# Optimization experiments

Measured on AMD Instinct MI355X. Metric: run time of the kernel, lower is better.

Reference implementation:

```python
import jax, jax.numpy as jnp
import numpy as np

H = 16  # text_transformer_heads


def setup_inputs() -> dict:
    key = jax.random.key(0)
    ks = jax.random.split(key, 5)
    B, T, D = 2, 2048, 1024
    std = D ** -0.5
    return {
        "x": jax.random.normal(ks[0], (B, T, D), dtype=jnp.float32),
        "wq": jax.random.normal(ks[1], (D, D), dtype=jnp.float32) * std,
        "bq": jnp.zeros((D,), dtype=jnp.float32),
        "wk": jax.random.normal(ks[2], (D, D), dtype=jnp.float32) * std,
        "bk": jnp.zeros((D,), dtype=jnp.float32),
        "wv": jax.random.normal(ks[3], (D, D), dtype=jnp.float32) * std,
        "bv": jnp.zeros((D,), dtype=jnp.float32),
        "wo": jax.random.normal(ks[4], (D, D), dtype=jnp.float32) * std,
        "bo": jnp.zeros((D,), dtype=jnp.float32),
    }


def reference(x, wq, bq, wk, bk, wv, bv, wo, bo):
    # Faithful to the original: masked_fill result was discarded in torch,
    # so NO causal mask is applied; scale is 1/sqrt(T) (seq len, not head dim).
    B, T, D = x.shape
    hd = D // H
    q = (x @ wq.T + bq).reshape(B, T, H, hd).transpose(0, 2, 1, 3)  # [B,H,T,hd]
    k = (x @ wk.T + bk).reshape(B, T, H, hd).transpose(0, 2, 1, 3)
    v = (x @ wv.T + bv).reshape(B, T, H, hd).transpose(0, 2, 1, 3)
    scores = jnp.einsum("bhqd,bhkd->bhqk", q, k) / jnp.sqrt(jnp.float32(T))
    attn = jax.nn.softmax(scores, axis=-1)
    ctx = jnp.einsum("bhqk,bhkd->bhqd", attn, v)
    ctx = ctx.transpose(0, 2, 1, 3).reshape(B, T, D)
    return ctx @ wo.T + bo
```

## Files before the change

### kernel.cpp

```cpp
#include <hip/hip_runtime.h>
#include <hip/hip_bf16.h>
#include <stdint.h>

typedef __bf16 bf16x8_t __attribute__((ext_vector_type(8)));
typedef float f32x4_t __attribute__((ext_vector_type(4)));

#define B_SZ 2
#define T_SZ 2048
#define D_SZ 1024
#define H_SZ 16
#define M_SZ 4096
#define QK_SCALE (0.02209708691207961f * 1.4426950408889634f)

__device__ __forceinline__ void gld_lds16(const void* g, void* l) {
  __builtin_amdgcn_global_load_lds(
      (const __attribute__((address_space(1))) unsigned int*)g,
      (__attribute__((address_space(3))) unsigned int*)l, 16, 0, 0);
}

__device__ __forceinline__ int xcd_swz(int bid, int nwg) {
  return (bid & 7) * (nwg >> 3) + (bid >> 3);
}

__global__ __launch_bounds__(256) void cast_all_k(
    const float* __restrict__ x, const float* __restrict__ wq,
    const float* __restrict__ wk, const float* __restrict__ wv,
    const float* __restrict__ wo, __hip_bfloat16* __restrict__ dst) {
  size_t i = ((size_t)blockIdx.x * 256 + threadIdx.x) * 4;
  if (i >= 8388608) return;
  const float* src;
  size_t off;
  if (i < 4194304) { src = x; off = i; }
  else {
    size_t r = i - 4194304;
    int s = (int)(r >> 20);
    off = r & 1048575;
    src = s == 0 ? wq : s == 1 ? wk : s == 2 ? wv : wo;
  }
  float4 v = *(const float4*)(src + off);
  __hip_bfloat16 h0 = __float2bfloat16(v.x), h1 = __float2bfloat16(v.y);
  __hip_bfloat16 h2 = __float2bfloat16(v.z), h3 = __float2bfloat16(v.w);
  ushort4 u;
  u.x = *(unsigned short*)&h0; u.y = *(unsigned short*)&h1;
  u.z = *(unsigned short*)&h2; u.w = *(unsigned short*)&h3;
  *(ushort4*)(dst + i) = u;
}

__device__ __forceinline__ void gemm_mainloop(
    const __hip_bfloat16* __restrict__ A, const __hip_bfloat16* __restrict__ W,
    int m0, int n0, __hip_bfloat16* a_lds, __hip_bfloat16* b_lds,
    f32x4_t (&acc)[4][4]) {
  const int tid = threadIdx.x;
  const int w = tid >> 6, l = tid & 63, lr = l & 15, lg = l >> 4;
  const int wm = w >> 1, wn = w & 1;
  const int c0 = tid, c1 = tid + 256;
  const int r0 = c0 >> 2, k0c = c0 & 3;
  const int r1 = c1 >> 2, k1c = c1 & 3;
  const __hip_bfloat16* ga0 = A + (size_t)(m0 + r0) * 1024 + 8 * (k0c ^ (r0 & 3));
  const __hip_bfloat16* ga1 = A + (size_t)(m0 + r1) * 1024 + 8 * (k1c ^ (r1 & 3));
  const __hip_bfloat16* gb0 = W + (size_t)(n0 + r0) * 1024 + 8 * (k0c ^ (r0 & 3));
  const __hip_bfloat16* gb1 = W + (size_t)(n0 + r1) * 1024 + 8 * (k1c ^ (r1 & 3));
  __hip_bfloat16* la0 = a_lds + w * 512;
  __hip_bfloat16* la1 = a_lds + 2048 + w * 512;
  __hip_bfloat16* lb0 = b_lds + w * 512;
  __hip_bfloat16* lb1 = b_lds + 2048 + w * 512;

  int aoff[4], boff[4];
#pragma unroll
  for (int f = 0; f < 4; ++f) {
    int ra = wm * 64 + f * 16 + lr;
    aoff[f] = ra * 32 + 8 * (lg ^ (ra & 3));
    int rb = wn * 64 + f * 16 + lr;
    boff[f] = rb * 32 + 8 * (lg ^ (rb & 3));
  }

  for (int kk = 0; kk < 1024; kk += 32) {
    gld_lds16(ga0 + kk, la0);
    gld_lds16(ga1 + kk, la1);
    gld_lds16(gb0 + kk, lb0);
    gld_lds16(gb1 + kk, lb1);
    __syncthreads();
    bf16x8_t af[4], bfr[4];
#pragma unroll
    for (int f = 0; f < 4; ++f) {
      af[f]  = *(const bf16x8_t*)(a_lds + aoff[f]);
      bfr[f] = *(const bf16x8_t*)(b_lds + boff[f]);
    }
#pragma unroll
    for (int i = 0; i < 4; ++i)
#pragma unroll
      for (int j = 0; j < 4; ++j)
        acc[i][j] = __builtin_amdgcn_mfma_f32_16x16x32_bf16(af[i], bfr[j], acc[i][j], 0, 0, 0);
    __syncthreads();
  }
}

__global__ __launch_bounds__(256, 2) void gemm_qkv(
    const __hip_bfloat16* __restrict__ xb,
    const __hip_bfloat16* __restrict__ wqb, const __hip_bfloat16* __restrict__ wkb,
    const __hip_bfloat16* __restrict__ wvb,
    const float* __restrict__ bq, const float* __restrict__ bk,
    const float* __restrict__ bv,
    __hip_bfloat16* __restrict__ qo, __hip_bfloat16* __restrict__ ko,
    __hip_bfloat16* __restrict__ vto) {
  __shared__ __hip_bfloat16 a_lds[4096];
  __shared__ __hip_bfloat16 b_lds[4096];
  const int lin = xcd_swz(blockIdx.y * 24 + blockIdx.x, 768);
  const int bx = lin % 24, by = lin / 24;
  const int n0g = bx * 128;
  const int m0  = by * 128;
  const int seg = n0g >> 10;
  const int n0  = n0g & 1023;
  const __hip_bfloat16* W = seg == 0 ? wqb : seg == 1 ? wkb : wvb;
  const float* bias = seg == 0 ? bq : seg == 1 ? bk : bv;

  f32x4_t acc[4][4] = {};
  gemm_mainloop(xb, W, m0, n0, a_lds, b_lds, acc);

  const int tid = threadIdx.x;
  const int w = tid >> 6, l = tid & 63, lr = l & 15, lg = l >> 4;
  const int wm = w >> 1, wn = w & 1;
#pragma unroll
  for (int i = 0; i < 4; ++i) {
#pragma unroll
    for (int j = 0; j < 4; ++j) {
      const int col = n0 + wn * 64 + j * 16 + lr;
      const float bb = bias[col];
      f32x4_t v = acc[i][j];
      const int row0 = m0 + wm * 64 + i * 16 + lg * 4;
      if (seg == 0) {
#pragma unroll
        for (int e = 0; e < 4; ++e)
          qo[(size_t)(row0 + e) * 1024 + col] = __float2bfloat16((v[e] + bb) * QK_SCALE);
      } else if (seg == 1) {
#pragma unroll
        for (int e = 0; e < 4; ++e)
          ko[(size_t)(row0 + e) * 1024 + col] = __float2bfloat16(v[e] + bb);
      } else {
        const int h = col >> 6, d = col & 63;
        const int b = row0 >> 11, t0 = row0 & 2047;
        union { unsigned short s[4]; uint2 u; } pk;
#pragma unroll
        for (int e = 0; e < 4; ++e) {
          __hip_bfloat16 hv = __float2bfloat16(v[e] + bb);
          pk.s[e] = *(unsigned short*)&hv;
        }
        *(uint2*)(vto + ((size_t)((b * 16 + h) * 64 + d)) * 2048 + t0) = pk.u;
      }
    }
  }
}

__global__ __launch_bounds__(512, 4) void attn_k(
    const __hip_bfloat16* __restrict__ q, const __hip_bfloat16* __restrict__ k,
    const __hip_bfloat16* __restrict__ vt, __hip_bfloat16* __restrict__ ctx) {
  __shared__ __hip_bfloat16 k_lds[2][4096];
  __shared__ __hip_bfloat16 v_lds[2][4096];
  __shared__ __hip_bfloat16 p_lds[8192];
  const int tid = threadIdx.x, w = tid >> 6, l = tid & 63;
  const int lr = l & 15, lg = l >> 4;
  const int bh = blockIdx.y, b = bh >> 4, h = bh & 15;
  const int q0 = blockIdx.x * 128;

  const int srow = tid >> 3, scc = tid & 7;
  const __hip_bfloat16* ksrc = k + ((size_t)(b * T_SZ + srow)) * 1024 + h * 64 + 8 * (scc ^ (srow & 7));
  const __hip_bfloat16* vsrc = vt + ((size_t)(bh * 64 + srow)) * 2048 + 8 * (scc ^ (srow & 7));
  __hip_bfloat16* kdst0 = &k_lds[0][0] + w * 512;
  __hip_bfloat16* kdst1 = &k_lds[1][0] + w * 512;
  __hip_bfloat16* vdst0 = &v_lds[0][0] + w * 512;
  __hip_bfloat16* vdst1 = &v_lds[1][0] + w * 512;
  __hip_bfloat16* pw = p_lds + w * 1024;

  gld_lds16(ksrc, kdst0);
  gld_lds16(vsrc, vdst0);

  const size_t qbase = ((size_t)(b * T_SZ + q0 + w * 16 + lr)) * 1024 + h * 64 + 8 * lg;
  const bf16x8_t aQ0 = *(const bf16x8_t*)(q + qbase);
  const bf16x8_t aQ1 = *(const bf16x8_t*)(q + qbase + 32);

  float mrow = -1e30f, lrow = 0.f;
  f32x4_t acc[4] = {};

  auto tile = [&](const __hip_bfloat16* kr, const __hip_bfloat16* vr,
                  bool pf, int tn, __hip_bfloat16* kd, __hip_bfloat16* vd) {
    if (pf) {
      gld_lds16(ksrc + (size_t)tn * 64 * 1024, kd);
      gld_lds16(vsrc + tn * 64, vd);
      asm volatile("s_waitcnt vmcnt(2)" ::: "memory");
    } else {
      asm volatile("s_waitcnt vmcnt(0)" ::: "memory");
    }
    __builtin_amdgcn_s_barrier();
    asm volatile("" ::: "memory");

    f32x4_t sf[4];
#pragma unroll
    for (int nt = 0; nt < 4; ++nt) {
      const int row = nt * 16 + lr;
      bf16x8_t b0 = *(const bf16x8_t*)(kr + row * 64 + 8 * (lg ^ (row & 7)));
      bf16x8_t b1 = *(const bf16x8_t*)(kr + row * 64 + 8 * ((lg + 4) ^ (row & 7)));
      f32x4_t s = {};
      s = __builtin_amdgcn_mfma_f32_16x16x32_bf16(b0, aQ0, s, 0, 0, 0);
      s = __builtin_amdgcn_mfma_f32_16x16x32_bf16(b1, aQ1, s, 0, 0, 0);
      sf[nt] = s;
    }

    float tmax = sf[0][0];
#pragma unroll
    for (int nt = 0; nt < 4; ++nt)
#pragma unroll
      for (int e = 0; e < 4; ++e) tmax = fmaxf(tmax, sf[nt][e]);
    tmax = fmaxf(tmax, __shfl_xor(tmax, 16));
    tmax = fmaxf(tmax, __shfl_xor(tmax, 32));
    const float newm = fmaxf(mrow, tmax);
    const float sc = __builtin_amdgcn_exp2f(mrow - newm);
    float rsum = 0.f;
#pragma unroll
    for (int nt = 0; nt < 4; ++nt)
#pragma unroll
      for (int e = 0; e < 4; ++e) {
        float p = __builtin_amdgcn_exp2f(sf[nt][e] - newm);
        sf[nt][e] = p;
        rsum += p;
      }
    rsum += __shfl_xor(rsum, 16);
    rsum += __shfl_xor(rsum, 32);
    lrow = lrow * sc + rsum;
    mrow = newm;

#pragma unroll
    for (int nt = 0; nt < 4; ++nt) {
      union { unsigned short s[4]; uint2 u; } pk;
#pragma unroll
      for (int e = 0; e < 4; ++e) {
        __hip_bfloat16 hv = __float2bfloat16(sf[nt][e]);
        pk.s[e] = *(unsigned short*)&hv;
      }
      const int off = lr * 64 + 8 * ((nt * 2 + (lg >> 1)) ^ (lr & 7)) + (lg & 1) * 4;
      *(uint2*)(pw + off) = pk.u;
    }

    float sce[4];
#pragma unroll
    for (int e = 0; e < 4; ++e) sce[e] = __shfl(sc, lg * 4 + e, 16);
#pragma unroll
    for (int dt = 0; dt < 4; ++dt)
#pragma unroll
      for (int e = 0; e < 4; ++e) acc[dt][e] *= sce[e];

    asm volatile("s_waitcnt lgkmcnt(0)" ::: "memory");
    const bf16x8_t aP0 = *(const bf16x8_t*)(pw + lr * 64 + 8 * (lg ^ (lr & 7)));
    const bf16x8_t aP1 = *(const bf16x8_t*)(pw + lr * 64 + 8 * ((lg + 4) ^ (lr & 7)));

#pragma unroll
    for (int dt = 0; dt < 4; ++dt) {
      const int drow = dt * 16 + lr;
      bf16x8_t bv0 = *(const bf16x8_t*)(vr + drow * 64 + 8 * (lg ^ (drow & 7)));
      bf16x8_t bv1 = *(const bf16x8_t*)(vr + drow * 64 + 8 * ((lg + 4) ^ (drow & 7)));
      acc[dt] = __builtin_amdgcn_mfma_f32_16x16x32_bf16(aP0, bv0, acc[dt], 0, 0, 0);
      acc[dt] = __builtin_amdgcn_mfma_f32_16x16x32_bf16(aP1, bv1, acc[dt], 0, 0, 0);
    }
    asm volatile("" ::: "memory");
    __builtin_amdgcn_s_barrier();
  };

  const __hip_bfloat16* kb0 = &k_lds[0][0];
  const __hip_bfloat16* kb1 = &k_lds[1][0];
  const __hip_bfloat16* vb0 = &v_lds[0][0];
  const __hip_bfloat16* vb1 = &v_lds[1][0];
#pragma unroll 1
  for (int p = 0; p < 16; ++p) {
    tile(kb0, vb0, true, 2 * p + 1, kdst1, vdst1);
    tile(kb1, vb1, p < 15, 2 * p + 2, kdst0, vdst0);
  }

  const float inv = 1.0f / lrow;
  float inve[4];
#pragma unroll
  for (int e = 0; e < 4; ++e) inve[e] = __shfl(inv, lg * 4 + e, 16);
#pragma unroll
  for (int e = 0; e < 4; ++e) {
    const int row = q0 + w * 16 + lg * 4 + e;
#pragma unroll
    for (int dt = 0; dt < 4; ++dt) {
      const int d = dt * 16 + lr;
      ctx[((size_t)(b * T_SZ + row)) * 1024 + h * 64 + d] =
          __float2bfloat16(acc[dt][e] * inve[e]);
    }
  }
}

__global__ __launch_bounds__(256, 2) void gemm_out(
    const __hip_bfloat16* __restrict__ ctx, const __hip_bfloat16* __restrict__ wob,
    const float* __restrict__ bo, float* __restrict__ out) {
  __shared__ __hip_bfloat16 a_lds[4096];
  __shared__ __hip_bfloat16 b_lds[4096];
  const int lin = xcd_swz(blockIdx.y * 8 + blockIdx.x, 256);
  const int n0 = (lin % 8) * 128, m0 = (lin / 8) * 128;
  f32x4_t acc[4][4] = {};
  gemm_mainloop(ctx, wob, m0, n0, a_lds, b_lds, acc);
  const int tid = threadIdx.x;
  const int w = tid >> 6, l = tid & 63, lr = l & 15, lg = l >> 4;
  const int wm = w >> 1, wn = w & 1;
#pragma unroll
  for (int i = 0; i < 4; ++i) {
#pragma unroll
    for (int j = 0; j < 4; ++j) {
      const int col = n0 + wn * 64 + j * 16 + lr;
      const float bb = bo[col];
      f32x4_t v = acc[i][j];
#pragma unroll
      for (int e = 0; e < 4; ++e) {
        const int row = m0 + wm * 64 + i * 16 + lg * 4 + e;
        out[(size_t)row * 1024 + col] = v[e] + bb;
      }
    }
  }
}

extern "C" void kernel_launch(void* const* d_in, const int* in_sizes, int n_in,
                              void* d_out, int out_size, void* d_ws, size_t ws_size,
                              hipStream_t stream) {
  const float* x  = (const float*)d_in[0];
  const float* wq = (const float*)d_in[1];
  const float* bq = (const float*)d_in[2];
  const float* wk = (const float*)d_in[3];
  const float* bk = (const float*)d_in[4];
  const float* wv = (const float*)d_in[5];
  const float* bv = (const float*)d_in[6];
  const float* wo = (const float*)d_in[7];
  const float* bo = (const float*)d_in[8];
  float* out = (float*)d_out;

  __hip_bfloat16* ws = (__hip_bfloat16*)d_ws;
  __hip_bfloat16* xb  = ws;
  __hip_bfloat16* wqb = xb + 4194304;
  __hip_bfloat16* wkb = wqb + 1048576;
  __hip_bfloat16* wvb = wkb + 1048576;
  __hip_bfloat16* wob = wvb + 1048576;
  __hip_bfloat16* qb  = wob + 1048576;
  __hip_bfloat16* kb  = qb + 4194304;
  __hip_bfloat16* vtb = kb + 4194304;
  __hip_bfloat16* ctxb = vtb + 4194304;

  cast_all_k<<<8192, 256, 0, stream>>>(x, wq, wk, wv, wo, xb);
  gemm_qkv<<<dim3(24, 32), 256, 0, stream>>>(xb, wqb, wkb, wvb, bq, bk, bv, qb, kb, vtb);
  attn_k<<<dim3(16, 32), 512, 0, stream>>>(qb, kb, vtb, ctxb);
  gemm_out<<<dim3(8, 32), 256, 0, stream>>>(ctxb, wob, bo, out);
}
```

Before: 208.3 us.

## Double-buffer LDS tiles in GEMM mainloop to overlap global loads with MFMA

The shared GEMM mainloop now keeps two LDS buffers per operand and issues the next k-tile's direct-to-LDS global loads before computing on the current one. It waits with a partial vmcnt(4) and raw s_barrier instead of a full __syncthreads. This is meant to hide global memory latency behind the MFMA work in the QKV and output projections, at the cost of doubled LDS per block. That extra LDS could limit occupancy.

```diff
diff --git a/kernel.cpp b/kernel.cpp
--- a/kernel.cpp
+++ b/kernel.cpp
@@ -60,10 +60,6 @@
   const __hip_bfloat16* ga1 = A + (size_t)(m0 + r1) * 1024 + 8 * (k1c ^ (r1 & 3));
   const __hip_bfloat16* gb0 = W + (size_t)(n0 + r0) * 1024 + 8 * (k0c ^ (r0 & 3));
   const __hip_bfloat16* gb1 = W + (size_t)(n0 + r1) * 1024 + 8 * (k1c ^ (r1 & 3));
-  __hip_bfloat16* la0 = a_lds + w * 512;
-  __hip_bfloat16* la1 = a_lds + 2048 + w * 512;
-  __hip_bfloat16* lb0 = b_lds + w * 512;
-  __hip_bfloat16* lb1 = b_lds + 2048 + w * 512;
 
   int aoff[4], boff[4];
 #pragma unroll
@@ -74,25 +70,44 @@
     boff[f] = rb * 32 + 8 * (lg ^ (rb & 3));
   }
 
-  for (int kk = 0; kk < 1024; kk += 32) {
-    gld_lds16(ga0 + kk, la0);
-    gld_lds16(ga1 + kk, la1);
-    gld_lds16(gb0 + kk, lb0);
-    gld_lds16(gb1 + kk, lb1);
-    __syncthreads();
+  auto STAGE = [&](int kk, int buf) {
+    __hip_bfloat16* la = a_lds + buf * 4096;
+    __hip_bfloat16* lb = b_lds + buf * 4096;
+    gld_lds16(ga0 + kk, la + w * 512);
+    gld_lds16(ga1 + kk, la + 2048 + w * 512);
+    gld_lds16(gb0 + kk, lb + w * 512);
+    gld_lds16(gb1 + kk, lb + 2048 + w * 512);
+  };
+  auto COMPUTE = [&](int buf) {
+    const __hip_bfloat16* la = a_lds + buf * 4096;
+    const __hip_bfloat16* lb = b_lds + buf * 4096;
     bf16x8_t af[4], bfr[4];
 #pragma unroll
     for (int f = 0; f < 4; ++f) {
-      af[f]  = *(const bf16x8_t*)(a_lds + aoff[f]);
-      bfr[f] = *(const bf16x8_t*)(b_lds + boff[f]);
+      af[f]  = *(const bf16x8_t*)(la + aoff[f]);
+      bfr[f] = *(const bf16x8_t*)(lb + boff[f]);
     }
 #pragma unroll
     for (int i = 0; i < 4; ++i)
 #pragma unroll
       for (int j = 0; j < 4; ++j)
         acc[i][j] = __builtin_amdgcn_mfma_f32_16x16x32_bf16(af[i], bfr[j], acc[i][j], 0, 0, 0);
-    __syncthreads();
-  }
+  };
+
+  STAGE(0, 0);
+  for (int t = 0; t < 31; ++t) {
+    STAGE((t + 1) * 32, (t + 1) & 1);
+    asm volatile("s_waitcnt vmcnt(4)" ::: "memory");
+    __builtin_amdgcn_s_barrier();
+    asm volatile("" ::: "memory");
+    COMPUTE(t & 1);
+    asm volatile("" ::: "memory");
+    __builtin_amdgcn_s_barrier();
+  }
+  asm volatile("s_waitcnt vmcnt(0)" ::: "memory");
+  __builtin_amdgcn_s_barrier();
+  asm volatile("" ::: "memory");
+  COMPUTE(1);
 }
 
 __global__ __launch_bounds__(256, 2) void gemm_qkv(
@@ -103,8 +118,8 @@
     const float* __restrict__ bv,
     __hip_bfloat16* __restrict__ qo, __hip_bfloat16* __restrict__ ko,
     __hip_bfloat16* __restrict__ vto) {
-  __shared__ __hip_bfloat16 a_lds[4096];
-  __shared__ __hip_bfloat16 b_lds[4096];
+  __shared__ __hip_bfloat16 a_lds[8192];
+  __shared__ __hip_bfloat16 b_lds[8192];
   const int lin = xcd_swz(blockIdx.y * 24 + blockIdx.x, 768);
   const int bx = lin % 24, by = lin / 24;
   const int n0g = bx * 128;
@@ -293,8 +308,8 @@
 __global__ __launch_bounds__(256, 2) void gemm_out(
     const __hip_bfloat16* __restrict__ ctx, const __hip_bfloat16* __restrict__ wob,
     const float* __restrict__ bo, float* __restrict__ out) {
-  __shared__ __hip_bfloat16 a_lds[4096];
-  __shared__ __hip_bfloat16 b_lds[4096];
+  __shared__ __hip_bfloat16 a_lds[8192];
+  __shared__ __hip_bfloat16 b_lds[8192];
   const int lin = xcd_swz(blockIdx.y * 8 + blockIdx.x, 256);
   const int n0 = (lin % 8) * 128, m0 = (lin / 8) * 128;
   f32x4_t acc[4][4] = {};
```

Result: faster. 204.0 us (-2.1%).
